# Optimization experiments

Measured on AMD Instinct MI355X. Metric: run time of the kernel, lower is better.

## Reference

```python
import jax, jax.numpy as jnp
import numpy as np

H = 16
D_MODEL = 1024
D_K = D_MODEL // H  # 64
NEG = -1e9


def setup_inputs() -> dict:
    key = jax.random.key(0)
    ks = jax.random.split(key, 9)
    nb, nw = 4, 2048
    Q = jax.random.normal(ks[0], (nb, nw, D_MODEL), dtype=jnp.float32)
    K = jax.random.normal(ks[1], (nb, nw, D_MODEL), dtype=jnp.float32)
    V = jax.random.normal(ks[2], (nb, nw, D_MODEL), dtype=jnp.float32)
    mask = jax.random.randint(ks[3], (nb, nw, nw), 0, 2, dtype=jnp.int32)
    s = 1.0 / np.sqrt(D_MODEL)
    Wq = jax.random.normal(ks[4], (D_MODEL, D_MODEL), dtype=jnp.float32) * s
    Wk = jax.random.normal(ks[5], (D_MODEL, D_MODEL), dtype=jnp.float32) * s
    Wv = jax.random.normal(ks[6], (D_MODEL, D_MODEL), dtype=jnp.float32) * s
    Wo = jax.random.normal(ks[7], (D_MODEL, D_MODEL), dtype=jnp.float32) * s
    return {"Q": Q, "K": K, "V": V, "mask": mask,
            "Wq": Wq, "Wk": Wk, "Wv": Wv, "Wo": Wo}


def reference(Q, K, V, mask, Wq, Wk, Wv, Wo):
    nb, nw, _ = Q.shape
    scaling = jnp.asarray(np.sqrt(D_K), dtype=Q.dtype)
    # nn.Linear(bias=False): y = x @ W.T; split heads -> [nb, h, nw, d_k]
    q = (Q @ Wq.T).reshape(nb, nw, H, D_K).transpose(0, 2, 1, 3)
    k = (K @ Wk.T).reshape(nb, nw, H, D_K).transpose(0, 2, 1, 3)
    v = (V @ Wv.T).reshape(nb, nw, H, D_K).transpose(0, 2, 1, 3)
    scores = jnp.einsum('bhqd,bhkd->bhqk', q, k) / scaling
    # mask broadcast over heads (unsqueeze(1) in torch)
    scores = jnp.where(mask[:, None, :, :] == 0, jnp.asarray(NEG, scores.dtype), scores)
    probs = jax.nn.softmax(scores, axis=-1)
    # dropout is identity in eval mode
    attn = jnp.einsum('bhqk,bhkd->bhqd', probs, v)
    x = attn.transpose(0, 2, 1, 3).reshape(nb, nw, D_MODEL)
    return x @ Wo.T
```

## Files before the change

### kernel.cpp

```cpp
#include <hip/hip_runtime.h>
#include <hip/hip_bf16.h>
#include <cstdint>
#include <cmath>

#define NB 4
#define NW 2048
#define DM 1024
#define NH 16
#define DK 64

typedef __attribute__((ext_vector_type(8))) short bf16x8;
typedef __attribute__((ext_vector_type(4))) float f32x4;
union cvt8 { uint4 u; __hip_bfloat16 h[8]; };
union pk2 { unsigned u; unsigned short s[2]; };

__device__ __forceinline__ void async_ld16(const void* g, void* l) {
  __builtin_amdgcn_global_load_lds((__attribute__((address_space(1))) void*)g,
                                   (__attribute__((address_space(3))) void*)l,
                                   16, 0, 0);
}

__device__ __forceinline__ unsigned short bf16bits(float x) {
  __hip_bfloat16 h = __float2bfloat16(x);
  return *(unsigned short*)&h;
}

__device__ __forceinline__ float exp2_fast(float x) {
  float r;
  asm("v_exp_f32 %0, %1" : "=v"(r) : "v"(x));
  return r;
}

__global__ void __launch_bounds__(256) cvt_qkv(const float* __restrict__ Q,
                                               const float* __restrict__ K,
                                               const float* __restrict__ V,
                                               __hip_bfloat16* __restrict__ Qb,
                                               __hip_bfloat16* __restrict__ Kb,
                                               __hip_bfloat16* __restrict__ Vb) {
  const float* in = blockIdx.y == 0 ? Q : (blockIdx.y == 1 ? K : V);
  __hip_bfloat16* out = blockIdx.y == 0 ? Qb : (blockIdx.y == 1 ? Kb : Vb);
  size_t i = ((size_t)blockIdx.x * 256 + threadIdx.x) * 8;
  float4 a = *(const float4*)(in + i);
  float4 b = *(const float4*)(in + i + 4);
  cvt8 c;
#pragma unroll
  for (int t = 0; t < 4; ++t) {
    c.h[t]     = __float2bfloat16(((const float*)&a)[t]);
    c.h[4 + t] = __float2bfloat16(((const float*)&b)[t]);
  }
  *(uint4*)(out + i) = c.u;
}

__global__ void __launch_bounds__(256) cvt_w(const float* __restrict__ W0,
                                             const float* __restrict__ W1,
                                             const float* __restrict__ W2,
                                             const float* __restrict__ W3,
                                             __hip_bfloat16* __restrict__ Wb) {
  const float* in = blockIdx.y == 0 ? W0 : (blockIdx.y == 1 ? W1 : (blockIdx.y == 2 ? W2 : W3));
  __hip_bfloat16* out = Wb + (size_t)blockIdx.y * DM * DM;
  size_t i = ((size_t)blockIdx.x * 256 + threadIdx.x) * 8;
  float4 a = *(const float4*)(in + i);
  float4 b = *(const float4*)(in + i + 4);
  cvt8 c;
#pragma unroll
  for (int t = 0; t < 4; ++t) {
    c.h[t]     = __float2bfloat16(((const float*)&a)[t]);
    c.h[4 + t] = __float2bfloat16(((const float*)&b)[t]);
  }
  *(uint4*)(out + i) = c.u;
}

__global__ void __launch_bounds__(256) mask_pack(const int* __restrict__ mask,
                                                 unsigned long long* __restrict__ bits) {
  int lane = threadIdx.x & 63;
  size_t tid = (size_t)blockIdx.x * blockDim.x + threadIdx.x;
  size_t widx = tid >> 6;
  int m = mask[widx * 64 + lane];
  unsigned long long bm = __ballot(m != 0);
  if (lane == 0) {
    int kt  = (int)(widx & 31);
    int row = (int)((widx >> 5) & 2047);
    int bb  = (int)(widx >> 16);
    bits[((size_t)bb * 32 + kt) * NW + row] = bm;
  }
}

__global__ void __launch_bounds__(256) gemm_qkv(const __hip_bfloat16* __restrict__ Qb,
                                                const __hip_bfloat16* __restrict__ Kb,
                                                const __hip_bfloat16* __restrict__ Vb,
                                                const __hip_bfloat16* __restrict__ Wb,
                                                __hip_bfloat16* __restrict__ q_ws,
                                                __hip_bfloat16* __restrict__ k_ws,
                                                __hip_bfloat16* __restrict__ vt) {
  __shared__ __align__(16) __hip_bfloat16 sA[128 * 32];
  __shared__ __align__(16) __hip_bfloat16 sB[128 * 32];
  const int z = blockIdx.z;
  const __hip_bfloat16* A = z == 0 ? Qb : (z == 1 ? Kb : Vb);
  const __hip_bfloat16* W = Wb + (size_t)z * DM * DM;
  const int tid = threadIdx.x;
  const int lane = tid & 63;
  const int l15 = lane & 15, quad = lane >> 4;
  const int rowA = blockIdx.y * 128;
  const int colB = blockIdx.x * 128;
  const int wm = ((tid >> 6) >> 1) * 64, wn = ((tid >> 6) & 1) * 64;

  const f32x4 fz = {0.f, 0.f, 0.f, 0.f};
  f32x4 acc[4][4];
#pragma unroll
  for (int i = 0; i < 4; ++i)
#pragma unroll
    for (int j = 0; j < 4; ++j) acc[i][j] = fz;

  for (int k0 = 0; k0 < DM; k0 += 32) {
#pragma unroll
    for (int j = 0; j < 2; ++j) {
      int c = j * 256 + tid;
      int r = c >> 2, col = (c & 3) * 8;
      int ldsOff = (j * 256 + (tid & ~63)) * 16;
      async_ld16(A + (size_t)(rowA + r) * DM + k0 + col, (char*)sA + ldsOff);
      async_ld16(W + (size_t)(colB + r) * DM + k0 + col, (char*)sB + ldsOff);
    }
    __syncthreads();
    bf16x8 af[4], bfr[4];
#pragma unroll
    for (int i = 0; i < 4; ++i) {
      af[i]  = *(const bf16x8*)(sA + (wm + i * 16 + l15) * 32 + quad * 8);
      bfr[i] = *(const bf16x8*)(sB + (wn + i * 16 + l15) * 32 + quad * 8);
    }
#pragma unroll
    for (int i = 0; i < 4; ++i)
#pragma unroll
      for (int j = 0; j < 4; ++j)
        acc[i][j] = __builtin_amdgcn_mfma_f32_16x16x32_bf16(af[i], bfr[j], acc[i][j], 0, 0, 0);
    __syncthreads();
  }

  if (z < 2) {
    __hip_bfloat16* C = z == 0 ? q_ws : k_ws;
    float alpha = z == 0 ? 0.18033688011112042f : 1.0f;
#pragma unroll
    for (int i = 0; i < 4; ++i) {
      int row = rowA + wm + i * 16 + quad * 4;
#pragma unroll
      for (int j = 0; j < 4; ++j) {
        int col = colB + wn + j * 16 + l15;
#pragma unroll
        for (int r = 0; r < 4; ++r)
          C[(size_t)(row + r) * DM + col] = __float2bfloat16(acc[i][j][r] * alpha);
      }
    }
  } else {
#pragma unroll
    for (int i = 0; i < 4; ++i) {
      int row = rowA + wm + i * 16 + quad * 4;
      int bb = row >> 11, tok = row & 2047;
#pragma unroll
      for (int j = 0; j < 4; ++j) {
        int col = colB + wn + j * 16 + l15;
        uint2 u;
        u.x = (unsigned int)bf16bits(acc[i][j][0]) | ((unsigned int)bf16bits(acc[i][j][1]) << 16);
        u.y = (unsigned int)bf16bits(acc[i][j][2]) | ((unsigned int)bf16bits(acc[i][j][3]) << 16);
        *(uint2*)(vt + ((size_t)bb * 1024 + col) * 2048 + tok) = u;
      }
    }
  }
}

__global__ void __launch_bounds__(256) gemm_out(const __hip_bfloat16* __restrict__ A,
                                                const __hip_bfloat16* __restrict__ W,
                                                float* __restrict__ C) {
  __shared__ __align__(16) __hip_bfloat16 sA[128 * 32];
  __shared__ __align__(16) __hip_bfloat16 sB[128 * 32];
  const int tid = threadIdx.x;
  const int lane = tid & 63;
  const int l15 = lane & 15, quad = lane >> 4;
  const int rowA = blockIdx.y * 128;
  const int colB = blockIdx.x * 128;
  const int wm = ((tid >> 6) >> 1) * 64, wn = ((tid >> 6) & 1) * 64;

  const f32x4 fz = {0.f, 0.f, 0.f, 0.f};
  f32x4 acc[4][4];
#pragma unroll
  for (int i = 0; i < 4; ++i)
#pragma unroll
    for (int j = 0; j < 4; ++j) acc[i][j] = fz;

  for (int k0 = 0; k0 < DM; k0 += 32) {
#pragma unroll
    for (int j = 0; j < 2; ++j) {
      int c = j * 256 + tid;
      int r = c >> 2, col = (c & 3) * 8;
      int ldsOff = (j * 256 + (tid & ~63)) * 16;
      async_ld16(A + (size_t)(rowA + r) * DM + k0 + col, (char*)sA + ldsOff);
      async_ld16(W + (size_t)(colB + r) * DM + k0 + col, (char*)sB + ldsOff);
    }
    __syncthreads();
    bf16x8 af[4], bfr[4];
#pragma unroll
    for (int i = 0; i < 4; ++i) {
      af[i]  = *(const bf16x8*)(sA + (wm + i * 16 + l15) * 32 + quad * 8);
      bfr[i] = *(const bf16x8*)(sB + (wn + i * 16 + l15) * 32 + quad * 8);
    }
#pragma unroll
    for (int i = 0; i < 4; ++i)
#pragma unroll
      for (int j = 0; j < 4; ++j)
        acc[i][j] = __builtin_amdgcn_mfma_f32_16x16x32_bf16(af[i], bfr[j], acc[i][j], 0, 0, 0);
    __syncthreads();
  }
#pragma unroll
  for (int i = 0; i < 4; ++i) {
    int row = rowA + wm + i * 16 + quad * 4;
#pragma unroll
    for (int j = 0; j < 4; ++j) {
      int col = colB + wn + j * 16 + l15;
#pragma unroll
      for (int r = 0; r < 4; ++r)
        C[(size_t)(row + r) * DM + col] = acc[i][j][r];
    }
  }
}

#define LDSK 72

__global__ void __launch_bounds__(256) attn_fused(const __hip_bfloat16* __restrict__ q,
                                                  const __hip_bfloat16* __restrict__ kk,
                                                  const __hip_bfloat16* __restrict__ vt,
                                                  const unsigned long long* __restrict__ mbt,
                                                  __hip_bfloat16* __restrict__ o) {
  __shared__ __align__(16) __hip_bfloat16 sK[64 * LDSK];
  __shared__ __align__(16) __hip_bfloat16 sVT[64 * LDSK];

  const int tid = threadIdx.x;
  const int wave = tid >> 6, lane = tid & 63;
  const int l15 = lane & 15, quad = lane >> 4;
  const int b = blockIdx.z, h = blockIdx.y;
  const int qbase = blockIdx.x * 64 + wave * 16;

  const __hip_bfloat16* qp = q + (size_t)(b * NW + qbase + l15) * DM + h * DK + quad * 8;
  bf16x8 aq0 = *(const bf16x8*)qp;
  bf16x8 aq1 = *(const bf16x8*)(qp + 32);

  const __hip_bfloat16* vbase = vt + ((size_t)b * 1024 + h * DK) * 2048;
  const unsigned long long* mrow = mbt + (size_t)b * 32 * NW + qbase + l15;

  const f32x4 fz = {0.f, 0.f, 0.f, 0.f};
  f32x4 oacc[4];
#pragma unroll
  for (int i = 0; i < 4; ++i) oacc[i] = fz;
  float lsr[4] = {0.f, 0.f, 0.f, 0.f};

  for (int kt = 0; kt < NW / 64; ++kt) {
    __syncthreads();
#pragma unroll
    for (int j = 0; j < 2; ++j) {
      int c = j * 256 + tid;
      int r = c >> 3, col = (c & 7) * 8;
      *(uint4*)(sK + r * LDSK + col) =
          *(const uint4*)(kk + (size_t)(b * NW + kt * 64 + r) * DM + h * DK + col);
      *(uint4*)(sVT + r * LDSK + col) =
          *(const uint4*)(vbase + (size_t)r * 2048 + kt * 64 + col);
    }
    unsigned long long mw = mrow[(size_t)kt * NW];
    __syncthreads();

    unsigned long long msh = mw >> (quad * 4);
    unsigned int u[4][2];
#pragma unroll
    for (int nc = 0; nc < 4; ++nc) {
      bf16x8 kf0 = *(const bf16x8*)(sK + (nc * 16 + l15) * LDSK + quad * 8);
      bf16x8 kf1 = *(const bf16x8*)(sK + (nc * 16 + l15) * LDSK + 32 + quad * 8);
      f32x4 t = fz;
      t = __builtin_amdgcn_mfma_f32_16x16x32_bf16(kf0, aq0, t, 0, 0, 0);
      t = __builtin_amdgcn_mfma_f32_16x16x32_bf16(kf1, aq1, t, 0, 0, 0);
      unsigned nib = (unsigned)(msh >> (nc * 16)) & 0xFu;
      float p[4];
#pragma unroll
      for (int r = 0; r < 4; ++r) {
        float e = exp2_fast(t[r]);
        if (!((nib >> r) & 1u)) e = 0.f;
        lsr[r] += e;
        p[r] = e;
      }
      pk2 w0; w0.s[0] = bf16bits(p[0]); w0.s[1] = bf16bits(p[1]); u[nc][0] = w0.u;
      pk2 w1; w1.s[0] = bf16bits(p[2]); w1.s[1] = bf16bits(p[3]); u[nc][1] = w1.u;
    }

    unsigned a0 = u[0][0], a2 = u[1][0];
    asm volatile("v_permlane32_swap_b32 %0, %1" : "+v"(a0), "+v"(a2));
    asm volatile("v_permlane16_swap_b32 %0, %1" : "+v"(a0), "+v"(a2));
    unsigned a1 = u[0][1], a3 = u[1][1];
    asm volatile("v_permlane32_swap_b32 %0, %1" : "+v"(a1), "+v"(a3));
    asm volatile("v_permlane16_swap_b32 %0, %1" : "+v"(a1), "+v"(a3));
    unsigned c0 = u[2][0], c2 = u[3][0];
    asm volatile("v_permlane32_swap_b32 %0, %1" : "+v"(c0), "+v"(c2));
    asm volatile("v_permlane16_swap_b32 %0, %1" : "+v"(c0), "+v"(c2));
    unsigned c1 = u[2][1], c3 = u[3][1];
    asm volatile("v_permlane32_swap_b32 %0, %1" : "+v"(c1), "+v"(c3));
    asm volatile("v_permlane16_swap_b32 %0, %1" : "+v"(c1), "+v"(c3));

    union { unsigned w[4]; bf16x8 v; } AP0, AP1;
    AP0.w[0] = a0; AP0.w[1] = a1; AP0.w[2] = a2; AP0.w[3] = a3;
    AP1.w[0] = c0; AP1.w[1] = c1; AP1.w[2] = c2; AP1.w[3] = c3;

#pragma unroll
    for (int nc = 0; nc < 4; ++nc) {
      bf16x8 vf0 = *(const bf16x8*)(sVT + (nc * 16 + l15) * LDSK + quad * 8);
      bf16x8 vf1 = *(const bf16x8*)(sVT + (nc * 16 + l15) * LDSK + 32 + quad * 8);
      oacc[nc] = __builtin_amdgcn_mfma_f32_16x16x32_bf16(AP0.v, vf0, oacc[nc], 0, 0, 0);
      oacc[nc] = __builtin_amdgcn_mfma_f32_16x16x32_bf16(AP1.v, vf1, oacc[nc], 0, 0, 0);
    }
  }

  float ls = (lsr[0] + lsr[1]) + (lsr[2] + lsr[3]);
  ls += __shfl_xor(ls, 16, 64);
  ls += __shfl_xor(ls, 32, 64);

  float inv[4];
#pragma unroll
  for (int r = 0; r < 4; ++r) {
    float lv = __shfl(ls, quad * 4 + r, 64);
    inv[r] = 1.0f / fmaxf(lv, 1e-30f);
  }
#pragma unroll
  for (int nc = 0; nc < 4; ++nc)
#pragma unroll
    for (int r = 0; r < 4; ++r)
      o[(size_t)(b * NW + qbase + quad * 4 + r) * DM + h * DK + nc * 16 + l15] =
          __float2bfloat16(oacc[nc][r] * inv[r]);
}

extern "C" void kernel_launch(void* const* d_in, const int* in_sizes, int n_in,
                              void* d_out, int out_size, void* d_ws, size_t ws_size,
                              hipStream_t stream) {
  const float* Q  = (const float*)d_in[0];
  const float* K  = (const float*)d_in[1];
  const float* V  = (const float*)d_in[2];
  const int*   Mm = (const int*)d_in[3];
  const float* Wq = (const float*)d_in[4];
  const float* Wk = (const float*)d_in[5];
  const float* Wv = (const float*)d_in[6];
  const float* Wo = (const float*)d_in[7];
  float* out = (float*)d_out;

  char* ws = (char*)d_ws;
  const size_t tb = (size_t)NB * NW * DM * sizeof(__hip_bfloat16);
  const size_t wb = (size_t)DM * DM * sizeof(__hip_bfloat16);
  __hip_bfloat16* Qb   = (__hip_bfloat16*)(ws);
  __hip_bfloat16* Kb   = (__hip_bfloat16*)(ws + tb);
  __hip_bfloat16* k_ws = (__hip_bfloat16*)(ws + 2 * tb);
  __hip_bfloat16* vt   = (__hip_bfloat16*)(ws + 3 * tb);
  __hip_bfloat16* Wb   = (__hip_bfloat16*)(ws + 4 * tb);
  unsigned long long* mbits = (unsigned long long*)(ws + 4 * tb + 4 * wb);
  __hip_bfloat16* q_ws = (__hip_bfloat16*)d_out;
  __hip_bfloat16* Vb   = (__hip_bfloat16*)((char*)d_out + tb);
  __hip_bfloat16* a_ws = Qb;

  const int gq = (int)((size_t)NB * NW * DM / 8 / 256);
  const int gw = (int)((size_t)DM * DM / 8 / 256);

  mask_pack<<<(size_t)NB * NW * NW / 256, 256, 0, stream>>>(Mm, mbits);
  cvt_qkv<<<dim3(gq, 3), 256, 0, stream>>>(Q, K, V, Qb, Kb, Vb);
  cvt_w<<<dim3(gw, 4), 256, 0, stream>>>(Wq, Wk, Wv, Wo, Wb);
  gemm_qkv<<<dim3(DM / 128, NB * NW / 128, 3), 256, 0, stream>>>(Qb, Kb, Vb, Wb,
                                                                 q_ws, k_ws, vt);
  attn_fused<<<dim3(NW / 64, NH, NB), 256, 0, stream>>>(q_ws, k_ws, vt, mbits, a_ws);
  gemm_out<<<dim3(DM / 128, NB * NW / 128), 256, 0, stream>>>(a_ws, Wb + 3 * (size_t)DM * DM, out);
}
```

Before: 480.2 us.

## Process two 16-row query groups per wave in fused attention

Each wave now handles 32 query rows (two 16-row MFMA groups) instead of 16, so each block covers 128 queries and the grid halves. Every K/V tile loaded into LDS and every K/V fragment read from LDS is reused for twice as many queries, which reduces global and LDS traffic per unit of work. In exchange, register use roughly doubles for the accumulators and probabilities, and the grid drops to 1024 blocks, which may lower occupancy.

```diff
diff --git a/kernel.cpp b/kernel.cpp
--- a/kernel.cpp
+++ b/kernel.cpp
@@ -235,20 +235,25 @@
   const int wave = tid >> 6, lane = tid & 63;
   const int l15 = lane & 15, quad = lane >> 4;
   const int b = blockIdx.z, h = blockIdx.y;
-  const int qbase = blockIdx.x * 64 + wave * 16;
+  const int qbase = blockIdx.x * 128 + wave * 32;
 
   const __hip_bfloat16* qp = q + (size_t)(b * NW + qbase + l15) * DM + h * DK + quad * 8;
   bf16x8 aq0 = *(const bf16x8*)qp;
   bf16x8 aq1 = *(const bf16x8*)(qp + 32);
+  bf16x8 aq2 = *(const bf16x8*)(qp + (size_t)16 * DM);
+  bf16x8 aq3 = *(const bf16x8*)(qp + (size_t)16 * DM + 32);
 
   const __hip_bfloat16* vbase = vt + ((size_t)b * 1024 + h * DK) * 2048;
   const unsigned long long* mrow = mbt + (size_t)b * 32 * NW + qbase + l15;
 
   const f32x4 fz = {0.f, 0.f, 0.f, 0.f};
-  f32x4 oacc[4];
-#pragma unroll
-  for (int i = 0; i < 4; ++i) oacc[i] = fz;
-  float lsr[4] = {0.f, 0.f, 0.f, 0.f};
+  f32x4 oacc[2][4];
+#pragma unroll
+  for (int g = 0; g < 2; ++g)
+#pragma unroll
+    for (int i = 0; i < 4; ++i) oacc[g][i] = fz;
+  float lsr0[4] = {0.f, 0.f, 0.f, 0.f};
+  float lsr1[4] = {0.f, 0.f, 0.f, 0.f};
 
   for (int kt = 0; kt < NW / 64; ++kt) {
     __syncthreads();
@@ -261,73 +266,97 @@
       *(uint4*)(sVT + r * LDSK + col) =
           *(const uint4*)(vbase + (size_t)r * 2048 + kt * 64 + col);
     }
-    unsigned long long mw = mrow[(size_t)kt * NW];
-    __syncthreads();
-
-    unsigned long long msh = mw >> (quad * 4);
-    unsigned int u[4][2];
+    unsigned long long mw0 = mrow[(size_t)kt * NW];
+    unsigned long long mw1 = mrow[(size_t)kt * NW + 16];
+    __syncthreads();
+
+    unsigned long long msh0 = mw0 >> (quad * 4);
+    unsigned long long msh1 = mw1 >> (quad * 4);
+    unsigned u0[4][2], u1[4][2];
 #pragma unroll
     for (int nc = 0; nc < 4; ++nc) {
       bf16x8 kf0 = *(const bf16x8*)(sK + (nc * 16 + l15) * LDSK + quad * 8);
       bf16x8 kf1 = *(const bf16x8*)(sK + (nc * 16 + l15) * LDSK + 32 + quad * 8);
-      f32x4 t = fz;
-      t = __builtin_amdgcn_mfma_f32_16x16x32_bf16(kf0, aq0, t, 0, 0, 0);
-      t = __builtin_amdgcn_mfma_f32_16x16x32_bf16(kf1, aq1, t, 0, 0, 0);
-      unsigned nib = (unsigned)(msh >> (nc * 16)) & 0xFu;
-      float p[4];
+      f32x4 t0 = fz, t1 = fz;
+      t0 = __builtin_amdgcn_mfma_f32_16x16x32_bf16(kf0, aq0, t0, 0, 0, 0);
+      t0 = __builtin_amdgcn_mfma_f32_16x16x32_bf16(kf1, aq1, t0, 0, 0, 0);
+      t1 = __builtin_amdgcn_mfma_f32_16x16x32_bf16(kf0, aq2, t1, 0, 0, 0);
+      t1 = __builtin_amdgcn_mfma_f32_16x16x32_bf16(kf1, aq3, t1, 0, 0, 0);
+      unsigned nib0 = (unsigned)(msh0 >> (nc * 16)) & 0xFu;
+      unsigned nib1 = (unsigned)(msh1 >> (nc * 16)) & 0xFu;
+      float p0[4], p1[4];
 #pragma unroll
       for (int r = 0; r < 4; ++r) {
-        float e = exp2_fast(t[r]);
-        if (!((nib >> r) & 1u)) e = 0.f;
-        lsr[r] += e;
-        p[r] = e;
+        float e0 = exp2_fast(t0[r]);
+        float e1 = exp2_fast(t1[r]);
+        if (!((nib0 >> r) & 1u)) e0 = 0.f;
+        if (!((nib1 >> r) & 1u)) e1 = 0.f;
+        lsr0[r] += e0;
+        lsr1[r] += e1;
+        p0[r] = e0;
+        p1[r] = e1;
       }
-      pk2 w0; w0.s[0] = bf16bits(p[0]); w0.s[1] = bf16bits(p[1]); u[nc][0] = w0.u;
-      pk2 w1; w1.s[0] = bf16bits(p[2]); w1.s[1] = bf16bits(p[3]); u[nc][1] = w1.u;
-    }
-
-    unsigned a0 = u[0][0], a2 = u[1][0];
-    asm volatile("v_permlane32_swap_b32 %0, %1" : "+v"(a0), "+v"(a2));
-    asm volatile("v_permlane16_swap_b32 %0, %1" : "+v"(a0), "+v"(a2));
-    unsigned a1 = u[0][1], a3 = u[1][1];
-    asm volatile("v_permlane32_swap_b32 %0, %1" : "+v"(a1), "+v"(a3));
-    asm volatile("v_permlane16_swap_b32 %0, %1" : "+v"(a1), "+v"(a3));
-    unsigned c0 = u[2][0], c2 = u[3][0];
-    asm volatile("v_permlane32_swap_b32 %0, %1" : "+v"(c0), "+v"(c2));
-    asm volatile("v_permlane16_swap_b32 %0, %1" : "+v"(c0), "+v"(c2));
-    unsigned c1 = u[2][1], c3 = u[3][1];
-    asm volatile("v_permlane32_swap_b32 %0, %1" : "+v"(c1), "+v"(c3));
-    asm volatile("v_permlane16_swap_b32 %0, %1" : "+v"(c1), "+v"(c3));
-
-    union { unsigned w[4]; bf16x8 v; } AP0, AP1;
-    AP0.w[0] = a0; AP0.w[1] = a1; AP0.w[2] = a2; AP0.w[3] = a3;
-    AP1.w[0] = c0; AP1.w[1] = c1; AP1.w[2] = c2; AP1.w[3] = c3;
+      pk2 w;
+      w.s[0] = bf16bits(p0[0]); w.s[1] = bf16bits(p0[1]); u0[nc][0] = w.u;
+      w.s[0] = bf16bits(p0[2]); w.s[1] = bf16bits(p0[3]); u0[nc][1] = w.u;
+      w.s[0] = bf16bits(p1[0]); w.s[1] = bf16bits(p1[1]); u1[nc][0] = w.u;
+      w.s[0] = bf16bits(p1[2]); w.s[1] = bf16bits(p1[3]); u1[nc][1] = w.u;
+    }
+
+#define PERM2(x, y)                                                  \
+    asm volatile("v_permlane32_swap_b32 %0, %1" : "+v"(x), "+v"(y)); \
+    asm volatile("v_permlane16_swap_b32 %0, %1" : "+v"(x), "+v"(y));
+    unsigned g0a0 = u0[0][0], g0a2 = u0[1][0]; PERM2(g0a0, g0a2)
+    unsigned g0a1 = u0[0][1], g0a3 = u0[1][1]; PERM2(g0a1, g0a3)
+    unsigned g0c0 = u0[2][0], g0c2 = u0[3][0]; PERM2(g0c0, g0c2)
+    unsigned g0c1 = u0[2][1], g0c3 = u0[3][1]; PERM2(g0c1, g0c3)
+    unsigned g1a0 = u1[0][0], g1a2 = u1[1][0]; PERM2(g1a0, g1a2)
+    unsigned g1a1 = u1[0][1], g1a3 = u1[1][1]; PERM2(g1a1, g1a3)
+    unsigned g1c0 = u1[2][0], g1c2 = u1[3][0]; PERM2(g1c0, g1c2)
+    unsigned g1c1 = u1[2][1], g1c3 = u1[3][1]; PERM2(g1c1, g1c3)
+#undef PERM2
+
+    union { unsigned w[4]; bf16x8 v; } A00, A01, A10, A11;
+    A00.w[0] = g0a0; A00.w[1] = g0a1; A00.w[2] = g0a2; A00.w[3] = g0a3;
+    A01.w[0] = g0c0; A01.w[1] = g0c1; A01.w[2] = g0c2; A01.w[3] = g0c3;
+    A10.w[0] = g1a0; A10.w[1] = g1a1; A10.w[2] = g1a2; A10.w[3] = g1a3;
+    A11.w[0] = g1c0; A11.w[1] = g1c1; A11.w[2] = g1c2; A11.w[3] = g1c3;
 
 #pragma unroll
     for (int nc = 0; nc < 4; ++nc) {
       bf16x8 vf0 = *(const bf16x8*)(sVT + (nc * 16 + l15) * LDSK + quad * 8);
       bf16x8 vf1 = *(const bf16x8*)(sVT + (nc * 16 + l15) * LDSK + 32 + quad * 8);
-      oacc[nc] = __builtin_amdgcn_mfma_f32_16x16x32_bf16(AP0.v, vf0, oacc[nc], 0, 0, 0);
-      oacc[nc] = __builtin_amdgcn_mfma_f32_16x16x32_bf16(AP1.v, vf1, oacc[nc], 0, 0, 0);
-    }
-  }
-
-  float ls = (lsr[0] + lsr[1]) + (lsr[2] + lsr[3]);
-  ls += __shfl_xor(ls, 16, 64);
-  ls += __shfl_xor(ls, 32, 64);
-
-  float inv[4];
+      oacc[0][nc] = __builtin_amdgcn_mfma_f32_16x16x32_bf16(A00.v, vf0, oacc[0][nc], 0, 0, 0);
+      oacc[0][nc] = __builtin_amdgcn_mfma_f32_16x16x32_bf16(A01.v, vf1, oacc[0][nc], 0, 0, 0);
+      oacc[1][nc] = __builtin_amdgcn_mfma_f32_16x16x32_bf16(A10.v, vf0, oacc[1][nc], 0, 0, 0);
+      oacc[1][nc] = __builtin_amdgcn_mfma_f32_16x16x32_bf16(A11.v, vf1, oacc[1][nc], 0, 0, 0);
+    }
+  }
+
+  float ls0 = (lsr0[0] + lsr0[1]) + (lsr0[2] + lsr0[3]);
+  ls0 += __shfl_xor(ls0, 16, 64);
+  ls0 += __shfl_xor(ls0, 32, 64);
+  float ls1 = (lsr1[0] + lsr1[1]) + (lsr1[2] + lsr1[3]);
+  ls1 += __shfl_xor(ls1, 16, 64);
+  ls1 += __shfl_xor(ls1, 32, 64);
+
+  float inv0[4], inv1[4];
 #pragma unroll
   for (int r = 0; r < 4; ++r) {
-    float lv = __shfl(ls, quad * 4 + r, 64);
-    inv[r] = 1.0f / fmaxf(lv, 1e-30f);
+    float lv0 = __shfl(ls0, quad * 4 + r, 64);
+    float lv1 = __shfl(ls1, quad * 4 + r, 64);
+    inv0[r] = 1.0f / fmaxf(lv0, 1e-30f);
+    inv1[r] = 1.0f / fmaxf(lv1, 1e-30f);
   }
 #pragma unroll
   for (int nc = 0; nc < 4; ++nc)
 #pragma unroll
-    for (int r = 0; r < 4; ++r)
+    for (int r = 0; r < 4; ++r) {
       o[(size_t)(b * NW + qbase + quad * 4 + r) * DM + h * DK + nc * 16 + l15] =
-          __float2bfloat16(oacc[nc][r] * inv[r]);
+          __float2bfloat16(oacc[0][nc][r] * inv0[r]);
+      o[(size_t)(b * NW + qbase + 16 + quad * 4 + r) * DM + h * DK + nc * 16 + l15] =
+          __float2bfloat16(oacc[1][nc][r] * inv1[r]);
+    }
 }
 
 extern "C" void kernel_launch(void* const* d_in, const int* in_sizes, int n_in,
@@ -364,6 +393,6 @@
   cvt_w<<<dim3(gw, 4), 256, 0, stream>>>(Wq, Wk, Wv, Wo, Wb);
   gemm_qkv<<<dim3(DM / 128, NB * NW / 128, 3), 256, 0, stream>>>(Qb, Kb, Vb, Wb,
                                                                  q_ws, k_ws, vt);
-  attn_fused<<<dim3(NW / 64, NH, NB), 256, 0, stream>>>(q_ws, k_ws, vt, mbits, a_ws);
+  attn_fused<<<dim3(NW / 128, NH, NB), 256, 0, stream>>>(q_ws, k_ws, vt, mbits, a_ws);
   gemm_out<<<dim3(DM / 128, NB * NW / 128), 256, 0, stream>>>(a_ws, Wb + 3 * (size_t)DM * DM, out);
 }
```

Result: slower. 495.4 us (+3.2%).
